# Performance work log

Measured on AMD Instinct MI355X. Metric: run time of the kernel, lower is better.

The kernel has to match this reference:

```python
import jax, jax.numpy as jnp
import numpy as np

EMB_DIM = 2048
NUM_HEADS = 16
HEAD_DIM = EMB_DIM // NUM_HEADS  # 128
B, T = 4, 2048


def setup_inputs() -> dict:
    key = jax.random.key(0)
    ks = jax.random.split(key, 6)
    s = lambda fan_in: 1.0 / np.sqrt(fan_in)
    return {
        "x": jax.random.normal(ks[0], (B, T, EMB_DIM), dtype=jnp.float32),
        # weights stored [in, out] so forward is x @ W
        "Wq": jax.random.normal(ks[1], (EMB_DIM, EMB_DIM), dtype=jnp.float32) * s(EMB_DIM),
        "Wk": jax.random.normal(ks[2], (EMB_DIM, HEAD_DIM), dtype=jnp.float32) * s(EMB_DIM),
        "Wv": jax.random.normal(ks[3], (EMB_DIM, HEAD_DIM), dtype=jnp.float32) * s(EMB_DIM),
        "Wo": jax.random.normal(ks[4], (EMB_DIM, EMB_DIM), dtype=jnp.float32) * s(EMB_DIM),
        "bo": jax.random.normal(ks[5], (EMB_DIM,), dtype=jnp.float32) * 0.01,
    }


def reference(x, Wq, Wk, Wv, Wo, bo):
    Bsz, Tlen, C = x.shape
    H, D = NUM_HEADS, HEAD_DIM
    q = (x @ Wq).reshape(Bsz, Tlen, H, D)          # [B,T,H,D]
    k = x @ Wk                                      # [B,T,D] (single shared head)
    v = x @ Wv                                      # [B,T,D]
    # MQA: K/V broadcast over heads via einsum (no expand materialization)
    scores = jnp.einsum("bihd,bjd->bhij", q, k) / jnp.sqrt(jnp.float32(D))
    i = jnp.arange(Tlen)[:, None]
    j = jnp.arange(Tlen)[None, :]
    causal = j <= i                                  # attend to past & self
    scores = jnp.where(causal, scores, -jnp.inf)
    attn = jax.nn.softmax(scores, axis=-1)           # [B,H,T,T]
    out = jnp.einsum("bhij,bjd->bihd", attn, v).reshape(Bsz, Tlen, C)
    return out @ Wo + bo
```

## Files before the change

### kernel.cpp

```cpp
#include <hip/hip_runtime.h>
#include <stdint.h>

typedef __attribute__((ext_vector_type(8))) short short8;
typedef __attribute__((ext_vector_type(4))) float floatx4;

#define TLEN 2048
#define BATCH 4
#define EMB 2048
#define NHEADS 16
#define HDIM 128
#define MROWS (BATCH * TLEN)
#define QTILES (TLEN / 64)

__device__ __forceinline__ ushort f2bf(float f) {
    union { float f; uint32_t u; } v; v.f = f;
    uint32_t u = v.u;
    return (ushort)((u + 0x7fffu + ((u >> 16) & 1u)) >> 16);
}

__device__ __forceinline__ void async_copy16(const ushort* g, ushort* l) {
    __builtin_amdgcn_global_load_lds(
        (const __attribute__((address_space(1))) uint32_t*)g,
        (__attribute__((address_space(3))) uint32_t*)l, 16, 0, 0);
}

__global__ __launch_bounds__(256) void cast_bf16_kernel(const float* __restrict__ in,
                                                        ushort* __restrict__ out, int n) {
    int i = (blockIdx.x * 256 + threadIdx.x) * 4;
    if (i >= n) return;
    float4 f = *(const float4*)(in + i);
    ushort4 o;
    o.x = f2bf(f.x); o.y = f2bf(f.y); o.z = f2bf(f.z); o.w = f2bf(f.w);
    *(ushort4*)(out + i) = o;
}

__global__ void transpose_cast_kernel(const float* __restrict__ in, ushort* __restrict__ out,
                                      int R, int Cc) {
    __shared__ float tile[32][33];
    int x = blockIdx.x * 32 + threadIdx.x;
    int y0 = blockIdx.y * 32;
#pragma unroll
    for (int i = 0; i < 4; i++) {
        int y = y0 + threadIdx.y + i * 8;
        tile[threadIdx.y + i * 8][threadIdx.x] = in[(size_t)y * Cc + x];
    }
    __syncthreads();
    int xo = y0 + threadIdx.x;
#pragma unroll
    for (int i = 0; i < 4; i++) {
        int yo = blockIdx.x * 32 + threadIdx.y + i * 8;
        out[(size_t)yo * R + xo] = f2bf(tile[threadIdx.x][threadIdx.y + i * 8]);
    }
}

template <int MODE>
__global__ __launch_bounds__(256) void gemm_bt_kernel(const ushort* __restrict__ A,
                                                      const ushort* __restrict__ Bt,
                                                      void* __restrict__ Cp,
                                                      void* __restrict__ Cp2,
                                                      const float* __restrict__ bias,
                                                      int M, int N, int K) {
    __shared__ ushort As[128 * 64];
    __shared__ ushort Bs[128 * 64];
    int tid = threadIdx.x;
    int wid = tid >> 6, lane = tid & 63;
    int quad = lane >> 4, l15 = lane & 15;
    int m0 = blockIdx.y * 128;
    int n0 = blockIdx.x * 128;
    int rm = (wid >> 1) * 64;
    int cn = (wid & 1) * 64;
    int grow = lane >> 3;
    int gcol = (lane & 7) * 8;

    floatx4 acc[4][4];
#pragma unroll
    for (int i = 0; i < 4; i++)
#pragma unroll
        for (int j = 0; j < 4; j++)
#pragma unroll
            for (int r = 0; r < 4; r++) acc[i][j][r] = 0.f;

    for (int kk = 0; kk < K; kk += 64) {
#pragma unroll
        for (int c = 0; c < 4; c++) {
            int chunk = wid * 4 + c;
            int row = chunk * 8 + grow;
            async_copy16(A + (size_t)(m0 + row) * K + kk + gcol, &As[chunk * 512]);
            async_copy16(Bt + (size_t)(n0 + row) * K + kk + gcol, &Bs[chunk * 512]);
        }
        __syncthreads();
#pragma unroll
        for (int ks = 0; ks < 64; ks += 32) {
            short8 af[4], bf[4];
#pragma unroll
            for (int i = 0; i < 4; i++)
                af[i] = *(const short8*)(&As[(rm + i * 16 + l15) * 64 + ks + quad * 8]);
#pragma unroll
            for (int j = 0; j < 4; j++)
                bf[j] = *(const short8*)(&Bs[(cn + j * 16 + l15) * 64 + ks + quad * 8]);
#pragma unroll
            for (int i = 0; i < 4; i++)
#pragma unroll
                for (int j = 0; j < 4; j++)
                    acc[i][j] = __builtin_amdgcn_mfma_f32_16x16x32_bf16(af[i], bf[j], acc[i][j], 0, 0, 0);
        }
        __syncthreads();
    }
#pragma unroll
    for (int i = 0; i < 4; i++)
#pragma unroll
        for (int j = 0; j < 4; j++) {
            if (MODE == 2 && n0 != 0) {
                int d = cn + j * 16 + l15;
                int row = m0 + rm + i * 16 + quad * 4;
                ushort4 o;
                o.x = f2bf(acc[i][j][0]); o.y = f2bf(acc[i][j][1]);
                o.z = f2bf(acc[i][j][2]); o.w = f2bf(acc[i][j][3]);
                *(ushort4*)((ushort*)Cp2 + (size_t)d * M + row) = o;
            } else {
#pragma unroll
                for (int r = 0; r < 4; r++) {
                    int row = m0 + rm + i * 16 + quad * 4 + r;
                    int col = n0 + cn + j * 16 + l15;
                    float v = acc[i][j][r];
                    if (MODE == 0) {
                        ((ushort*)Cp)[(size_t)row * N + col] = f2bf(v);
                    } else if (MODE == 1) {
                        ((float*)Cp)[(size_t)row * N + col] = v + bias[col];
                    } else {
                        ((ushort*)Cp)[(size_t)row * HDIM + col] = f2bf(v);
                    }
                }
            }
        }
}

__global__ __launch_bounds__(256, 2) void mqa_attn_kernel(const ushort* __restrict__ Qb,
                                                          const ushort* __restrict__ Kb,
                                                          const ushort* __restrict__ Vg,
                                                          ushort* __restrict__ Ab) {
    __shared__ ushort Ks[64][136];
    __shared__ ushort Vs[128][72];
    __shared__ ushort Ps[4][2][16][72];
    int tid = threadIdx.x;
    int wid = tid >> 6, lane = tid & 63;
    int quad = lane >> 4, l15 = lane & 15;
    int h0 = blockIdx.y * 2, b = blockIdx.z;
    const float scale2 = 0.08838834764831845f * 1.4426950408889634f;
    const ushort* kbase0 = Kb + (size_t)b * TLEN * HDIM;
    const ushort* vbase0 = Vg + (size_t)b * TLEN;

#pragma unroll 1
    for (int t = 0; t < 2; t++) {
        int qt = (t == 0) ? blockIdx.x : (QTILES - 1 - blockIdx.x);
        size_t qrowbase = (size_t)b * TLEN + qt * 64;

        short8 aq[2][4];
#pragma unroll
        for (int hh = 0; hh < 2; hh++) {
            const ushort* qp = Qb + (qrowbase + wid * 16 + l15) * EMB + (h0 + hh) * HDIM + quad * 8;
#pragma unroll
            for (int kd = 0; kd < 4; kd++) aq[hh][kd] = *(const short8*)(qp + kd * 32);
        }

        float lsum[2];
        floatx4 o_acc[2][8];
#pragma unroll
        for (int hh = 0; hh < 2; hh++) {
            lsum[hh] = 0.f;
#pragma unroll
            for (int nd = 0; nd < 8; nd++)
#pragma unroll
                for (int r = 0; r < 4; r++) o_acc[hh][nd][r] = 0.f;
        }

        uint4 kreg[4], vreg[4];
#pragma unroll
        for (int it = 0; it < 4; it++) {
            int idx = tid + it * 256;
            kreg[it] = *(const uint4*)(kbase0 + (size_t)(idx >> 4) * HDIM + (idx & 15) * 8);
            vreg[it] = *(const uint4*)(vbase0 + (size_t)(idx >> 3) * MROWS + (idx & 7) * 8);
        }

#pragma unroll 1
        for (int jt = 0; jt <= qt; ++jt) {
#pragma unroll
            for (int it = 0; it < 4; it++) {
                int idx = tid + it * 256;
                *(uint4*)(&Ks[idx >> 4][(idx & 15) * 8]) = kreg[it];
                *(uint4*)(&Vs[idx >> 3][(idx & 7) * 8]) = vreg[it];
            }
            __syncthreads();
            if (jt < qt) {
                const ushort* kb = kbase0 + (size_t)(jt + 1) * 64 * HDIM;
                const ushort* vb = vbase0 + (jt + 1) * 64;
#pragma unroll
                for (int it = 0; it < 4; it++) {
                    int idx = tid + it * 256;
                    kreg[it] = *(const uint4*)(kb + (size_t)(idx >> 4) * HDIM + (idx & 15) * 8);
                    vreg[it] = *(const uint4*)(vb + (size_t)(idx >> 3) * MROWS + (idx & 7) * 8);
                }
            }

            floatx4 sacc[2][4];
#pragma unroll
            for (int hh = 0; hh < 2; hh++)
#pragma unroll
                for (int j = 0; j < 4; j++)
#pragma unroll
                    for (int r = 0; r < 4; r++) sacc[hh][j][r] = 0.f;
            __builtin_amdgcn_s_setprio(1);
#pragma unroll
            for (int kd = 0; kd < 4; kd++)
#pragma unroll
                for (int j = 0; j < 4; j++) {
                    short8 ak = *(const short8*)(&Ks[j * 16 + l15][kd * 32 + quad * 8]);
                    sacc[0][j] = __builtin_amdgcn_mfma_f32_16x16x32_bf16(ak, aq[0][kd], sacc[0][j], 0, 0, 0);
                    sacc[1][j] = __builtin_amdgcn_mfma_f32_16x16x32_bf16(ak, aq[1][kd], sacc[1][j], 0, 0, 0);
                }
            __builtin_amdgcn_s_setprio(0);

            int rowloc = wid * 16 + l15;
            bool diag = (jt == qt);
#pragma unroll
            for (int hh = 0; hh < 2; hh++) {
#pragma unroll
                for (int j = 0; j < 4; j++) {
                    float e[4];
#pragma unroll
                    for (int r = 0; r < 4; r++) {
                        float ev = exp2f(sacc[hh][j][r] * scale2);
                        if (diag && (j * 16 + quad * 4 + r) > rowloc) ev = 0.f;
                        e[r] = ev;
                        lsum[hh] += ev;
                    }
                    ushort4 pk;
                    pk.x = f2bf(e[0]); pk.y = f2bf(e[1]);
                    pk.z = f2bf(e[2]); pk.w = f2bf(e[3]);
                    *(ushort4*)(&Ps[wid][hh][l15][j * 16 + quad * 4]) = pk;
                }
            }

            __builtin_amdgcn_s_setprio(1);
#pragma unroll
            for (int kt = 0; kt < 2; kt++) {
                short8 pf0 = *(const short8*)(&Ps[wid][0][l15][kt * 32 + quad * 8]);
                short8 pf1 = *(const short8*)(&Ps[wid][1][l15][kt * 32 + quad * 8]);
#pragma unroll
                for (int nd = 0; nd < 8; nd++) {
                    short8 vf = *(const short8*)(&Vs[nd * 16 + l15][kt * 32 + quad * 8]);
                    o_acc[0][nd] = __builtin_amdgcn_mfma_f32_16x16x32_bf16(pf0, vf, o_acc[0][nd], 0, 0, 0);
                    o_acc[1][nd] = __builtin_amdgcn_mfma_f32_16x16x32_bf16(pf1, vf, o_acc[1][nd], 0, 0, 0);
                }
            }
            __builtin_amdgcn_s_setprio(0);
            __syncthreads();
        }

#pragma unroll
        for (int hh = 0; hh < 2; hh++) {
            float ls = lsum[hh];
            ls += __shfl_xor(ls, 16);
            ls += __shfl_xor(ls, 32);
            float inv_l[4];
#pragma unroll
            for (int r = 0; r < 4; r++) inv_l[r] = 1.f / __shfl(ls, quad * 4 + r, 16);
#pragma unroll
            for (int nd = 0; nd < 8; nd++)
#pragma unroll
                for (int r = 0; r < 4; r++) {
                    size_t row = qrowbase + wid * 16 + quad * 4 + r;
                    int col = (h0 + hh) * HDIM + nd * 16 + l15;
                    Ab[row * EMB + col] = f2bf(o_acc[hh][nd][r] * inv_l[r]);
                }
        }
    }
}

extern "C" void kernel_launch(void* const* d_in, const int* in_sizes, int n_in,
                              void* d_out, int out_size, void* d_ws, size_t ws_size,
                              hipStream_t stream) {
    const float* x  = (const float*)d_in[0];
    const float* Wq = (const float*)d_in[1];
    const float* Wk = (const float*)d_in[2];
    const float* Wv = (const float*)d_in[3];
    const float* Wo = (const float*)d_in[4];
    const float* bo = (const float*)d_in[5];
    float* out = (float*)d_out;

    ushort* ws = (ushort*)d_ws;
    ushort* Xb    = ws;
    ushort* Wq_t  = Xb    + (size_t)MROWS * EMB;
    ushort* Wkv_t = Wq_t  + (size_t)EMB * EMB;
    ushort* Wo_t  = Wkv_t + (size_t)256 * EMB;
    ushort* Qb    = Wo_t  + (size_t)EMB * EMB;
    ushort* Kb    = Qb    + (size_t)MROWS * EMB;
    ushort* Vg    = Kb    + (size_t)MROWS * HDIM;
    ushort* Ab    = Vg    + (size_t)HDIM * MROWS;

    cast_bf16_kernel<<<dim3(MROWS * EMB / 1024), 256, 0, stream>>>(x, Xb, MROWS * EMB);
    transpose_cast_kernel<<<dim3(EMB / 32, EMB / 32), dim3(32, 8), 0, stream>>>(Wq, Wq_t, EMB, EMB);
    transpose_cast_kernel<<<dim3(HDIM / 32, EMB / 32), dim3(32, 8), 0, stream>>>(Wk, Wkv_t, EMB, HDIM);
    transpose_cast_kernel<<<dim3(HDIM / 32, EMB / 32), dim3(32, 8), 0, stream>>>(Wv, Wkv_t + (size_t)HDIM * EMB, EMB, HDIM);
    transpose_cast_kernel<<<dim3(EMB / 32, EMB / 32), dim3(32, 8), 0, stream>>>(Wo, Wo_t, EMB, EMB);

    gemm_bt_kernel<0><<<dim3(EMB / 128, MROWS / 128), 256, 0, stream>>>(Xb, Wq_t, Qb, nullptr, nullptr, MROWS, EMB, EMB);
    gemm_bt_kernel<2><<<dim3(2, MROWS / 128), 256, 0, stream>>>(Xb, Wkv_t, Kb, Vg, nullptr, MROWS, 256, EMB);
    mqa_attn_kernel<<<dim3(QTILES / 2, NHEADS / 2, BATCH), 256, 0, stream>>>(Qb, Kb, Vg, Ab);
    gemm_bt_kernel<1><<<dim3(EMB / 128, MROWS / 128), 256, 0, stream>>>(Ab, Wo_t, out, nullptr, bo, MROWS, EMB, EMB);
}
```

Measured before the change: 577.4 us.

## Restructure MQA attention: one q-tile per block, async LDS loads, register P

The attention kernel now handles a single query tile per block instead of a paired short/long tile, and launches twice as many blocks with heaviest tiles first. K/V tiles go straight to LDS through global_load_lds with an XOR swizzle, replacing the register-staged prefetch. The P matrix stays in registers via cvt_pk_bf16 and permlane swaps, removing the Ps shared buffer, and the occupancy hint rises to 4 blocks per CU. The price is losing the overlap of the next tile's load with compute, since loads are now issued and waited on each iteration, plus some load imbalance risk.

```diff
diff --git a/kernel.cpp b/kernel.cpp
--- a/kernel.cpp
+++ b/kernel.cpp
@@ -16,6 +16,12 @@
     union { float f; uint32_t u; } v; v.f = f;
     uint32_t u = v.u;
     return (ushort)((u + 0x7fffu + ((u >> 16) & 1u)) >> 16);
+}
+
+__device__ __forceinline__ uint32_t cvt_pk_bf16(float a, float b) {
+    uint32_t r;
+    asm volatile("v_cvt_pk_bf16_f32 %0, %1, %2" : "=v"(r) : "v"(a), "v"(b));
+    return r;
 }
 
 __device__ __forceinline__ void async_copy16(const ushort* g, ushort* l) {
@@ -135,145 +141,128 @@
         }
 }
 
-__global__ __launch_bounds__(256, 2) void mqa_attn_kernel(const ushort* __restrict__ Qb,
+__global__ __launch_bounds__(256, 4) void mqa_attn_kernel(const ushort* __restrict__ Qb,
                                                           const ushort* __restrict__ Kb,
                                                           const ushort* __restrict__ Vg,
                                                           ushort* __restrict__ Ab) {
-    __shared__ ushort Ks[64][136];
-    __shared__ ushort Vs[128][72];
-    __shared__ ushort Ps[4][2][16][72];
+    __shared__ ushort Ks[64 * 128];
+    __shared__ ushort Vs[128 * 64];
     int tid = threadIdx.x;
     int wid = tid >> 6, lane = tid & 63;
     int quad = lane >> 4, l15 = lane & 15;
     int h0 = blockIdx.y * 2, b = blockIdx.z;
+    int qt = (QTILES - 1) - blockIdx.x;
     const float scale2 = 0.08838834764831845f * 1.4426950408889634f;
-    const ushort* kbase0 = Kb + (size_t)b * TLEN * HDIM;
-    const ushort* vbase0 = Vg + (size_t)b * TLEN;
+    const ushort* kbase = Kb + (size_t)b * TLEN * HDIM;
+    const ushort* vbase = Vg + (size_t)b * TLEN;
+    size_t qrowbase = (size_t)b * TLEN + qt * 64;
+
+    short8 aq[2][4];
+#pragma unroll
+    for (int hh = 0; hh < 2; hh++) {
+        const ushort* qp = Qb + (qrowbase + wid * 16 + l15) * EMB + (h0 + hh) * HDIM + quad * 8;
+#pragma unroll
+        for (int kd = 0; kd < 4; kd++) aq[hh][kd] = *(const short8*)(qp + kd * 32);
+    }
+
+    float lsum[2] = {0.f, 0.f};
+    floatx4 o_acc[2][8];
+#pragma unroll
+    for (int hh = 0; hh < 2; hh++)
+#pragma unroll
+        for (int nd = 0; nd < 8; nd++)
+#pragma unroll
+            for (int r = 0; r < 4; r++) o_acc[hh][nd][r] = 0.f;
+
+    int rowloc = wid * 16 + l15;
+    int swz = (l15 & 7) << 3;
 
 #pragma unroll 1
-    for (int t = 0; t < 2; t++) {
-        int qt = (t == 0) ? blockIdx.x : (QTILES - 1 - blockIdx.x);
-        size_t qrowbase = (size_t)b * TLEN + qt * 64;
-
-        short8 aq[2][4];
-#pragma unroll
-        for (int hh = 0; hh < 2; hh++) {
-            const ushort* qp = Qb + (qrowbase + wid * 16 + l15) * EMB + (h0 + hh) * HDIM + quad * 8;
-#pragma unroll
-            for (int kd = 0; kd < 4; kd++) aq[hh][kd] = *(const short8*)(qp + kd * 32);
-        }
-
-        float lsum[2];
-        floatx4 o_acc[2][8];
-#pragma unroll
-        for (int hh = 0; hh < 2; hh++) {
-            lsum[hh] = 0.f;
-#pragma unroll
-            for (int nd = 0; nd < 8; nd++)
-#pragma unroll
-                for (int r = 0; r < 4; r++) o_acc[hh][nd][r] = 0.f;
-        }
-
-        uint4 kreg[4], vreg[4];
-#pragma unroll
-        for (int it = 0; it < 4; it++) {
-            int idx = tid + it * 256;
-            kreg[it] = *(const uint4*)(kbase0 + (size_t)(idx >> 4) * HDIM + (idx & 15) * 8);
-            vreg[it] = *(const uint4*)(vbase0 + (size_t)(idx >> 3) * MROWS + (idx & 7) * 8);
-        }
-
-#pragma unroll 1
-        for (int jt = 0; jt <= qt; ++jt) {
-#pragma unroll
-            for (int it = 0; it < 4; it++) {
-                int idx = tid + it * 256;
-                *(uint4*)(&Ks[idx >> 4][(idx & 15) * 8]) = kreg[it];
-                *(uint4*)(&Vs[idx >> 3][(idx & 7) * 8]) = vreg[it];
-            }
-            __syncthreads();
-            if (jt < qt) {
-                const ushort* kb = kbase0 + (size_t)(jt + 1) * 64 * HDIM;
-                const ushort* vb = vbase0 + (jt + 1) * 64;
-#pragma unroll
-                for (int it = 0; it < 4; it++) {
-                    int idx = tid + it * 256;
-                    kreg[it] = *(const uint4*)(kb + (size_t)(idx >> 4) * HDIM + (idx & 15) * 8);
-                    vreg[it] = *(const uint4*)(vb + (size_t)(idx >> 3) * MROWS + (idx & 7) * 8);
+    for (int jt = 0; jt <= qt; ++jt) {
+#pragma unroll
+        for (int i = 0; i < 4; i++) {
+            int c = wid * 4 + i;
+            int kr = c * 4 + (lane >> 4);
+            int kc = ((lane & 15) * 8) ^ ((kr & 7) << 3);
+            async_copy16(kbase + (size_t)(jt * 64 + kr) * HDIM + kc, &Ks[c * 512]);
+            int vd = c * 8 + (lane >> 3);
+            int vc = ((lane & 7) * 8) ^ ((lane >> 3) << 3);
+            async_copy16(vbase + (size_t)vd * MROWS + jt * 64 + vc, &Vs[c * 512]);
+        }
+        __syncthreads();
+
+        bool diag = (jt == qt);
+#pragma unroll
+        for (int jp = 0; jp < 2; jp++) {
+            uint32_t XA[2][2], XB[2][2];
+#pragma unroll
+            for (int jj = 0; jj < 2; jj++) {
+                int j = jp * 2 + jj;
+                floatx4 s0, s1;
+#pragma unroll
+                for (int r = 0; r < 4; r++) { s0[r] = 0.f; s1[r] = 0.f; }
+                __builtin_amdgcn_s_setprio(1);
+#pragma unroll
+                for (int kd = 0; kd < 4; kd++) {
+                    short8 ak = *(const short8*)(&Ks[(j * 16 + l15) * 128 + ((kd * 32 + quad * 8) ^ swz)]);
+                    s0 = __builtin_amdgcn_mfma_f32_16x16x32_bf16(ak, aq[0][kd], s0, 0, 0, 0);
+                    s1 = __builtin_amdgcn_mfma_f32_16x16x32_bf16(ak, aq[1][kd], s1, 0, 0, 0);
                 }
-            }
-
-            floatx4 sacc[2][4];
-#pragma unroll
-            for (int hh = 0; hh < 2; hh++)
-#pragma unroll
-                for (int j = 0; j < 4; j++)
-#pragma unroll
-                    for (int r = 0; r < 4; r++) sacc[hh][j][r] = 0.f;
+                __builtin_amdgcn_s_setprio(0);
+                float e0[4], e1[4];
+#pragma unroll
+                for (int r = 0; r < 4; r++) {
+                    int key = j * 16 + quad * 4 + r;
+                    float v0 = exp2f(s0[r] * scale2);
+                    float v1 = exp2f(s1[r] * scale2);
+                    if (diag && key > rowloc) { v0 = 0.f; v1 = 0.f; }
+                    e0[r] = v0; e1[r] = v1;
+                    lsum[0] += v0; lsum[1] += v1;
+                }
+                XA[0][jj] = cvt_pk_bf16(e0[0], e0[1]); XB[0][jj] = cvt_pk_bf16(e0[2], e0[3]);
+                XA[1][jj] = cvt_pk_bf16(e1[0], e1[1]); XB[1][jj] = cvt_pk_bf16(e1[2], e1[3]);
+            }
+            short8 pf[2];
+#pragma unroll
+            for (int hh = 0; hh < 2; hh++) {
+                uint32_t xA = XA[hh][0], yA = XA[hh][1];
+                uint32_t xB = XB[hh][0], yB = XB[hh][1];
+                asm volatile("v_permlane32_swap_b32 %0, %1" : "+v"(xA), "+v"(yA));
+                asm volatile("v_permlane16_swap_b32 %0, %1" : "+v"(xA), "+v"(yA));
+                asm volatile("v_permlane32_swap_b32 %0, %1" : "+v"(xB), "+v"(yB));
+                asm volatile("v_permlane16_swap_b32 %0, %1" : "+v"(xB), "+v"(yB));
+                union { uint32_t u[4]; short8 s; } fu;
+                fu.u[0] = xA; fu.u[1] = xB; fu.u[2] = yA; fu.u[3] = yB;
+                pf[hh] = fu.s;
+            }
             __builtin_amdgcn_s_setprio(1);
 #pragma unroll
-            for (int kd = 0; kd < 4; kd++)
-#pragma unroll
-                for (int j = 0; j < 4; j++) {
-                    short8 ak = *(const short8*)(&Ks[j * 16 + l15][kd * 32 + quad * 8]);
-                    sacc[0][j] = __builtin_amdgcn_mfma_f32_16x16x32_bf16(ak, aq[0][kd], sacc[0][j], 0, 0, 0);
-                    sacc[1][j] = __builtin_amdgcn_mfma_f32_16x16x32_bf16(ak, aq[1][kd], sacc[1][j], 0, 0, 0);
-                }
+            for (int nd = 0; nd < 8; nd++) {
+                short8 vf = *(const short8*)(&Vs[(nd * 16 + l15) * 64 + ((jp * 32 + quad * 8) ^ swz)]);
+                o_acc[0][nd] = __builtin_amdgcn_mfma_f32_16x16x32_bf16(pf[0], vf, o_acc[0][nd], 0, 0, 0);
+                o_acc[1][nd] = __builtin_amdgcn_mfma_f32_16x16x32_bf16(pf[1], vf, o_acc[1][nd], 0, 0, 0);
+            }
             __builtin_amdgcn_s_setprio(0);
-
-            int rowloc = wid * 16 + l15;
-            bool diag = (jt == qt);
-#pragma unroll
-            for (int hh = 0; hh < 2; hh++) {
-#pragma unroll
-                for (int j = 0; j < 4; j++) {
-                    float e[4];
-#pragma unroll
-                    for (int r = 0; r < 4; r++) {
-                        float ev = exp2f(sacc[hh][j][r] * scale2);
-                        if (diag && (j * 16 + quad * 4 + r) > rowloc) ev = 0.f;
-                        e[r] = ev;
-                        lsum[hh] += ev;
-                    }
-                    ushort4 pk;
-                    pk.x = f2bf(e[0]); pk.y = f2bf(e[1]);
-                    pk.z = f2bf(e[2]); pk.w = f2bf(e[3]);
-                    *(ushort4*)(&Ps[wid][hh][l15][j * 16 + quad * 4]) = pk;
-                }
-            }
-
-            __builtin_amdgcn_s_setprio(1);
-#pragma unroll
-            for (int kt = 0; kt < 2; kt++) {
-                short8 pf0 = *(const short8*)(&Ps[wid][0][l15][kt * 32 + quad * 8]);
-                short8 pf1 = *(const short8*)(&Ps[wid][1][l15][kt * 32 + quad * 8]);
-#pragma unroll
-                for (int nd = 0; nd < 8; nd++) {
-                    short8 vf = *(const short8*)(&Vs[nd * 16 + l15][kt * 32 + quad * 8]);
-                    o_acc[0][nd] = __builtin_amdgcn_mfma_f32_16x16x32_bf16(pf0, vf, o_acc[0][nd], 0, 0, 0);
-                    o_acc[1][nd] = __builtin_amdgcn_mfma_f32_16x16x32_bf16(pf1, vf, o_acc[1][nd], 0, 0, 0);
-                }
-            }
-            __builtin_amdgcn_s_setprio(0);
-            __syncthreads();
-        }
-
-#pragma unroll
-        for (int hh = 0; hh < 2; hh++) {
-            float ls = lsum[hh];
-            ls += __shfl_xor(ls, 16);
-            ls += __shfl_xor(ls, 32);
-            float inv_l[4];
-#pragma unroll
-            for (int r = 0; r < 4; r++) inv_l[r] = 1.f / __shfl(ls, quad * 4 + r, 16);
-#pragma unroll
-            for (int nd = 0; nd < 8; nd++)
-#pragma unroll
-                for (int r = 0; r < 4; r++) {
-                    size_t row = qrowbase + wid * 16 + quad * 4 + r;
-                    int col = (h0 + hh) * HDIM + nd * 16 + l15;
-                    Ab[row * EMB + col] = f2bf(o_acc[hh][nd][r] * inv_l[r]);
-                }
-        }
+        }
+        __syncthreads();
+    }
+
+#pragma unroll
+    for (int hh = 0; hh < 2; hh++) {
+        float ls = lsum[hh];
+        ls += __shfl_xor(ls, 16);
+        ls += __shfl_xor(ls, 32);
+        float inv_l[4];
+#pragma unroll
+        for (int r = 0; r < 4; r++) inv_l[r] = 1.f / __shfl(ls, quad * 4 + r, 16);
+#pragma unroll
+        for (int nd = 0; nd < 8; nd++)
+#pragma unroll
+            for (int r = 0; r < 4; r++) {
+                size_t row = qrowbase + wid * 16 + quad * 4 + r;
+                int col = (h0 + hh) * HDIM + nd * 16 + l15;
+                Ab[row * EMB + col] = f2bf(o_acc[hh][nd][r] * inv_l[r]);
+            }
     }
 }
 
@@ -306,6 +295,6 @@
 
     gemm_bt_kernel<0><<<dim3(EMB / 128, MROWS / 128), 256, 0, stream>>>(Xb, Wq_t, Qb, nullptr, nullptr, MROWS, EMB, EMB);
     gemm_bt_kernel<2><<<dim3(2, MROWS / 128), 256, 0, stream>>>(Xb, Wkv_t, Kb, Vg, nullptr, MROWS, 256, EMB);
-    mqa_attn_kernel<<<dim3(QTILES / 2, NHEADS / 2, BATCH), 256, 0, stream>>>(Qb, Kb, Vg, Ab);
+    mqa_attn_kernel<<<dim3(QTILES, NHEADS / 2, BATCH), 256, 0, stream>>>(Qb, Kb, Vg, Ab);
     gemm_bt_kernel<1><<<dim3(EMB / 128, MROWS / 128), 256, 0, stream>>>(Ab, Wo_t, out, nullptr, bo, MROWS, EMB, EMB);
 }
```

Measured after the change: 557.1 us. 3.5% less time.
